# Kernel optimization log

Hardware: AMD Instinct MI355X
Metric: run time of the kernel (lower is better)

The kernel has to match this reference:

```python
import jax, jax.numpy as jnp
import numpy as np

EMBED_DIM = 1024
NUM_HEADS = 16
HEAD_DIM = EMBED_DIM // NUM_HEADS
B, S = 4, 2048


def setup_inputs() -> dict:
    key = jax.random.key(0)
    ks = jax.random.split(key, 12)
    s = 1.0 / np.sqrt(EMBED_DIM)
    inp = {
        'q': jax.random.normal(ks[0], (B, S, EMBED_DIM), jnp.float32),
        'k': jax.random.normal(ks[1], (B, S, EMBED_DIM), jnp.float32),
        'v': jax.random.normal(ks[2], (B, S, EMBED_DIM), jnp.float32),
        'mask': jnp.tril(jnp.ones((S, S), jnp.int32))[None, None],  # [1,1,S,S] causal
        'Wq': jax.random.normal(ks[3], (EMBED_DIM, EMBED_DIM), jnp.float32) * s,
        'bq': jax.random.normal(ks[4], (EMBED_DIM,), jnp.float32) * s,
        'Wk': jax.random.normal(ks[5], (EMBED_DIM, EMBED_DIM), jnp.float32) * s,
        'bk': jax.random.normal(ks[6], (EMBED_DIM,), jnp.float32) * s,
        'Wv': jax.random.normal(ks[7], (EMBED_DIM, EMBED_DIM), jnp.float32) * s,
        'bv': jax.random.normal(ks[8], (EMBED_DIM,), jnp.float32) * s,
        'Wo': jax.random.normal(ks[9], (EMBED_DIM, EMBED_DIM), jnp.float32) * s,
        'bo': jax.random.normal(ks[10], (EMBED_DIM,), jnp.float32) * s,
    }
    return inp


def _split(x):
    b, s, _ = x.shape
    return x.reshape(b, s, NUM_HEADS, HEAD_DIM).transpose(0, 2, 1, 3)  # [b,h,s,d]


def reference(q, k, v, mask, Wq, bq, Wk, bk, Wv, bv, Wo, bo):
    # torch Linear: x @ W.T + b
    Q = _split(q @ Wq.T + bq)
    K = _split(k @ Wk.T + bk)
    V = _split(v @ Wv.T + bv)
    scores = jnp.einsum('bhqd,bhkd->bhqk', Q, K) / np.sqrt(HEAD_DIM).astype(np.float32)
    scores = jnp.where(mask == 0, jnp.float32(-1e9), scores)
    attn = jax.nn.softmax(scores, axis=-1)  # dropout p=0.0 -> identity
    out = jnp.einsum('bhqk,bhkd->bhqd', attn, V)
    out = out.transpose(0, 2, 1, 3).reshape(q.shape[0], q.shape[1], EMBED_DIM)
    return out @ Wo.T + bo
```

## Files before the change

### kernel.cpp

```cpp
#include <hip/hip_runtime.h>

#define SEQ   2048
#define EMB   1024
#define NH    16
#define HD    64
#define BATCH 4

typedef __attribute__((ext_vector_type(8))) short short8;
typedef __attribute__((ext_vector_type(4))) float floatx4;
typedef __attribute__((ext_vector_type(4))) uint uintx4;

static __device__ __forceinline__ ushort f2bf_rne(float x) {
  unsigned u = __float_as_uint(x);
  unsigned r = u + 0x7FFFu + ((u >> 16) & 1u);
  return (ushort)(r >> 16);
}
static __device__ __forceinline__ float bf2f(ushort h) {
  return __uint_as_float(((unsigned)h) << 16);
}

static __device__ __forceinline__ uint pk_bf16(float a, float b) {
  uint r;
  asm("v_cvt_pk_bf16_f32 %0, %1, %2" : "=v"(r) : "v"(a), "v"(b));
  return r;
}
static __device__ __forceinline__ void split_pair(float a, float b, uint& h,
                                                  uint& l) {
  h = pk_bf16(a, b);
  const float ha = __uint_as_float(h << 16);
  const float hb = __uint_as_float(h & 0xFFFF0000u);
  l = pk_bf16(a - ha, b - hb);
}

static __device__ __forceinline__ void load16(const void* g, void* l) {
  __builtin_amdgcn_global_load_lds(
      (const __attribute__((address_space(1))) unsigned int*)g,
      (__attribute__((address_space(3))) unsigned int*)l, 16, 0, 0);
}

static __device__ __forceinline__ int swz_off(int row, int kg) {
  return (row >> 1) * 128 + (((row & 1) << 2) + (kg ^ ((row >> 1) & 3))) * 16;
}

static __device__ __forceinline__ void stage_tile(const ushort* __restrict__ g,
                                                  int row0, int k0,
                                                  ushort* lds, int t) {
#pragma unroll
  for (int i = 0; i < 2; ++i) {
    const int slot = t + i * 256;
    const int line = slot >> 3, s = slot & 7;
    const int row = line * 2 + (s >> 2);
    const int c = (s & 3) ^ (line & 3);
    load16(g + (size_t)(row0 + row) * EMB + k0 + c * 8, lds + slot * 8);
  }
}

static __device__ __forceinline__ void wconv_body(const float* W, ushort* Yh,
                                                  ushort* Yl, int bid, int t) {
  const int i = (bid * 256 + t) * 8;
  const float4 a = *(const float4*)(W + i);
  const float4 b = *(const float4*)(W + i + 4);
  const float xv[8] = {a.x, a.y, a.z, a.w, b.x, b.y, b.z, b.w};
  uintx4 H, L;
#pragma unroll
  for (int j = 0; j < 4; ++j) {
    uint h, l;
    split_pair(xv[2 * j], xv[2 * j + 1], h, l);
    H[j] = h;
    L[j] = l;
  }
  *(uintx4*)&Yh[i] = H;
  *(uintx4*)&Yl[i] = L;
}

__global__ __launch_bounds__(256) void wconv4_kernel(
    const float* __restrict__ Wq, const float* __restrict__ Wk,
    const float* __restrict__ Wv, const float* __restrict__ Wo,
    ushort* __restrict__ Yqh, ushort* __restrict__ Yql,
    ushort* __restrict__ Ykh, ushort* __restrict__ Ykl,
    ushort* __restrict__ Yvh, ushort* __restrict__ Yvl,
    ushort* __restrict__ Yoh, ushort* __restrict__ Yol) {
  const int which = blockIdx.x >> 9;
  const int bid = blockIdx.x & 511;
  const float* W = which == 0 ? Wq : which == 1 ? Wk : which == 2 ? Wv : Wo;
  ushort* Yh = which == 0 ? Yqh : which == 1 ? Ykh : which == 2 ? Yvh : Yoh;
  ushort* Yl = which == 0 ? Yql : which == 1 ? Ykl : which == 2 ? Yvl : Yol;
  wconv_body(W, Yh, Yl, bid, threadIdx.x);
}

__global__ __launch_bounds__(256) void wconv3_kernel(
    const float* __restrict__ Wq, const float* __restrict__ Wk,
    const float* __restrict__ Wv, ushort* __restrict__ Yqh,
    ushort* __restrict__ Yql, ushort* __restrict__ Ykh,
    ushort* __restrict__ Ykl, ushort* __restrict__ Yvh,
    ushort* __restrict__ Yvl) {
  const int which = blockIdx.x >> 9;
  const int bid = blockIdx.x & 511;
  const float* W = which == 0 ? Wq : which == 1 ? Wk : Wv;
  ushort* Yh = which == 0 ? Yqh : which == 1 ? Ykh : Yvh;
  ushort* Yl = which == 0 ? Yql : which == 1 ? Ykl : Yvl;
  wconv_body(W, Yh, Yl, bid, threadIdx.x);
}

__global__ __launch_bounds__(256) void wconv_kernel(const float* __restrict__ W,
                                                    ushort* __restrict__ Yh,
                                                    ushort* __restrict__ Yl) {
  wconv_body(W, Yh, Yl, blockIdx.x, threadIdx.x);
}

__global__ __launch_bounds__(256) void qkv_proj_kernel(
    const float* __restrict__ Xq, const float* __restrict__ Xk,
    const float* __restrict__ Xv, const ushort* __restrict__ Wqh,
    const ushort* __restrict__ Wql, const ushort* __restrict__ Wkh,
    const ushort* __restrict__ Wkl, const ushort* __restrict__ Wvh,
    const ushort* __restrict__ Wvl, const float* __restrict__ bq,
    const float* __restrict__ bk, const float* __restrict__ bv,
    ushort* __restrict__ Qh, ushort* __restrict__ Ql, ushort* __restrict__ Kh,
    ushort* __restrict__ Kl, ushort* __restrict__ Vth,
    ushort* __restrict__ Vtl) {
  __shared__ ushort Ahi[2][128 * 40], Alo[2][128 * 40];
  __shared__ ushort Bhi[2][128 * 32], Blo[2][128 * 32];

  const int mode = blockIdx.z;
  const float* X = mode == 0 ? Xq : mode == 1 ? Xk : Xv;
  const ushort* Wh = mode == 0 ? Wqh : mode == 1 ? Wkh : Wvh;
  const ushort* Wl = mode == 0 ? Wql : mode == 1 ? Wkl : Wvl;
  const float* bias = mode == 0 ? bq : mode == 1 ? bk : bv;
  ushort* Yh = mode == 0 ? Qh : mode == 1 ? Kh : Vth;
  ushort* Yl = mode == 0 ? Ql : mode == 1 ? Kl : Vtl;

  const int t = threadIdx.x;
  const int lane = t & 63, wave = t >> 6;
  const int m0 = blockIdx.y * 128, n0 = blockIdx.x * 128;
  const int wm = (wave >> 1) * 64, wn = (wave & 1) * 64;
  const int fr = lane & 15, kg = lane >> 4;

  floatx4 acc[4][4];
#pragma unroll
  for (int i = 0; i < 4; ++i)
#pragma unroll
    for (int j = 0; j < 4; ++j)
#pragma unroll
      for (int r = 0; r < 4; ++r) acc[i][j][r] = 0.f;

  auto stageB = [&](int k0, int b) {
    stage_tile(Wh, n0, k0, Bhi[b], t);
    stage_tile(Wl, n0, k0, Blo[b], t);
  };
  auto stageA = [&](int k0, int b) {
#pragma unroll
    for (int i = 0; i < 4; ++i) {
      const int f = t + 256 * i;
      const int row = f >> 3, kq = f & 7;
      const float4 v =
          *(const float4*)(X + (size_t)(m0 + row) * EMB + k0 + kq * 4);
      uint h0, l0, h1, l1;
      split_pair(v.x, v.y, h0, l0);
      split_pair(v.z, v.w, h1, l1);
      uint2 hp, lp;
      hp.x = h0; hp.y = h1;
      lp.x = l0; lp.y = l1;
      *(uint2*)&Ahi[b][row * 40 + kq * 4] = hp;
      *(uint2*)&Alo[b][row * 40 + kq * 4] = lp;
    }
  };
  auto computeStep = [&](int cur) {
    short8 bhv[4], blv[4];
#pragma unroll
    for (int nf = 0; nf < 4; ++nf) {
      const int row = wn + nf * 16 + fr;
      const int off = swz_off(row, kg);
      bhv[nf] = *(const short8*)((const char*)Bhi[cur] + off);
      blv[nf] = *(const short8*)((const char*)Blo[cur] + off);
    }
#pragma unroll
    for (int mf = 0; mf < 4; ++mf) {
      const int arow = wm + mf * 16 + fr;
      const short8 ah = *(const short8*)&Ahi[cur][arow * 40 + kg * 8];
      const short8 al = *(const short8*)&Alo[cur][arow * 40 + kg * 8];
#pragma unroll
      for (int nf = 0; nf < 4; ++nf) {
        acc[mf][nf] = __builtin_amdgcn_mfma_f32_16x16x32_bf16(ah, bhv[nf],
                                                              acc[mf][nf], 0, 0, 0);
        acc[mf][nf] = __builtin_amdgcn_mfma_f32_16x16x32_bf16(ah, blv[nf],
                                                              acc[mf][nf], 0, 0, 0);
        acc[mf][nf] = __builtin_amdgcn_mfma_f32_16x16x32_bf16(al, bhv[nf],
                                                              acc[mf][nf], 0, 0, 0);
      }
    }
  };

  stageB(0, 0);
  stageA(0, 0);
  asm volatile("s_waitcnt vmcnt(0)");
  __syncthreads();
#pragma unroll 1
  for (int k0 = 0; k0 < EMB; k0 += 32) {
    const int cur = (k0 >> 5) & 1;
    if (k0 + 32 < EMB) {
      stageB(k0 + 32, cur ^ 1);
      stageA(k0 + 32, cur ^ 1);
    }
    computeStep(cur);
    asm volatile("s_waitcnt vmcnt(0)");
    __syncthreads();
  }

  const int rg = lane >> 4;
#pragma unroll
  for (int nf = 0; nf < 4; ++nf) {
    const int n = n0 + wn + nf * 16 + fr;
    const float bb = bias[n];
    if (mode == 2) {
      const int hh = n >> 6, d = n & 63;
#pragma unroll
      for (int mf = 0; mf < 4; ++mf) {
        const int mb = m0 + wm + mf * 16 + rg * 4;
        const int b = mb >> 11, s = mb & (SEQ - 1);
        uint h0, l0, h1, l1;
        split_pair(acc[mf][nf][0] + bb, acc[mf][nf][1] + bb, h0, l0);
        split_pair(acc[mf][nf][2] + bb, acc[mf][nf][3] + bb, h1, l1);
        uint2 hp, lp;
        hp.x = h0; hp.y = h1;
        lp.x = l0; lp.y = l1;
        const int idx = (b * NH + hh) * (HD * SEQ) + d * SEQ + s;
        *(uint2*)&Yh[idx] = hp;
        *(uint2*)&Yl[idx] = lp;
      }
    } else {
      const float scaleq = (mode == 0) ? 0.125f : 1.0f;
#pragma unroll
      for (int mf = 0; mf < 4; ++mf) {
#pragma unroll
        for (int r = 0; r < 4; ++r) {
          const int m = m0 + wm + mf * 16 + rg * 4 + r;
          const float val = (acc[mf][nf][r] + bb) * scaleq;
          const int hh = n >> 6, d = n & 63;
          const int b = m >> 11, s = m & (SEQ - 1);
          const int idx = ((b * NH + hh) * SEQ + s) * HD + d;
          const ushort h = f2bf_rne(val);
          Yh[idx] = h;
          Yl[idx] = f2bf_rne(val - bf2f(h));
        }
      }
    }
  }
}

template <int MODE, bool PREA, bool PREB>
__global__ __launch_bounds__(256) void proj_mfma_kernel(
    const float* __restrict__ X, const ushort* __restrict__ Xh,
    const ushort* __restrict__ Xl, const float* __restrict__ W,
    const ushort* __restrict__ Wh, const ushort* __restrict__ Wl,
    const float* __restrict__ bias, float* __restrict__ Yf,
    ushort* __restrict__ Yh, ushort* __restrict__ Yl) {
  constexpr bool DBUF = (PREA || PREB);
  constexpr int NB = DBUF ? 2 : 1;
  constexpr int ASZ = PREA ? 128 * 32 : 128 * 40;
  constexpr int BSZ = PREB ? 128 * 32 : 128 * 40;
  __shared__ ushort Ahi[NB][ASZ], Alo[NB][ASZ];
  __shared__ ushort Bhi[NB][BSZ], Blo[NB][BSZ];

  const int t = threadIdx.x;
  const int lane = t & 63, wave = t >> 6;
  const int m0 = blockIdx.y * 128, n0 = blockIdx.x * 128;
  const int wm = (wave >> 1) * 64, wn = (wave & 1) * 64;
  const int fr = lane & 15, kg = lane >> 4;

  floatx4 acc[4][4];
#pragma unroll
  for (int i = 0; i < 4; ++i)
#pragma unroll
    for (int j = 0; j < 4; ++j)
#pragma unroll
      for (int r = 0; r < 4; ++r) acc[i][j][r] = 0.f;

  auto stageB = [&](int k0, int b) {
    if constexpr (PREB) {
      stage_tile(Wh, n0, k0, Bhi[b], t);
      stage_tile(Wl, n0, k0, Blo[b], t);
    } else {
#pragma unroll
      for (int i = 0; i < 4; ++i) {
        const int f = t + 256 * i;
        const int row = f >> 3, kq = f & 7;
        const float4 v =
            *(const float4*)(W + (size_t)(n0 + row) * EMB + k0 + kq * 4);
        uint h0, l0, h1, l1;
        split_pair(v.x, v.y, h0, l0);
        split_pair(v.z, v.w, h1, l1);
        uint2 hp, lp;
        hp.x = h0; hp.y = h1;
        lp.x = l0; lp.y = l1;
        *(uint2*)&Bhi[b][row * 40 + kq * 4] = hp;
        *(uint2*)&Blo[b][row * 40 + kq * 4] = lp;
      }
    }
  };
  auto stageA = [&](int k0, int b) {
    if constexpr (PREA) {
      stage_tile(Xh, m0, k0, Ahi[b], t);
      stage_tile(Xl, m0, k0, Alo[b], t);
    } else {
#pragma unroll
      for (int i = 0; i < 4; ++i) {
        const int f = t + 256 * i;
        const int row = f >> 3, kq = f & 7;
        const float4 v =
            *(const float4*)(X + (size_t)(m0 + row) * EMB + k0 + kq * 4);
        uint h0, l0, h1, l1;
        split_pair(v.x, v.y, h0, l0);
        split_pair(v.z, v.w, h1, l1);
        uint2 hp, lp;
        hp.x = h0; hp.y = h1;
        lp.x = l0; lp.y = l1;
        *(uint2*)&Ahi[b][row * 40 + kq * 4] = hp;
        *(uint2*)&Alo[b][row * 40 + kq * 4] = lp;
      }
    }
  };
  auto computeStep = [&](int cur) {
    short8 bhv[4], blv[4];
#pragma unroll
    for (int nf = 0; nf < 4; ++nf) {
      const int row = wn + nf * 16 + fr;
      if constexpr (PREB) {
        const int off = swz_off(row, kg);
        bhv[nf] = *(const short8*)((const char*)Bhi[cur] + off);
        blv[nf] = *(const short8*)((const char*)Blo[cur] + off);
      } else {
        bhv[nf] = *(const short8*)&Bhi[cur][row * 40 + kg * 8];
        blv[nf] = *(const short8*)&Blo[cur][row * 40 + kg * 8];
      }
    }
#pragma unroll
    for (int mf = 0; mf < 4; ++mf) {
      const int arow = wm + mf * 16 + fr;
      short8 ah, al;
      if constexpr (PREA) {
        const int off = swz_off(arow, kg);
        ah = *(const short8*)((const char*)Ahi[cur] + off);
        al = *(const short8*)((const char*)Alo[cur] + off);
      } else {
        ah = *(const short8*)&Ahi[cur][arow * 40 + kg * 8];
        al = *(const short8*)&Alo[cur][arow * 40 + kg * 8];
      }
#pragma unroll
      for (int nf = 0; nf < 4; ++nf) {
        acc[mf][nf] = __builtin_amdgcn_mfma_f32_16x16x32_bf16(ah, bhv[nf],
                                                              acc[mf][nf], 0, 0, 0);
        acc[mf][nf] = __builtin_amdgcn_mfma_f32_16x16x32_bf16(ah, blv[nf],
                                                              acc[mf][nf], 0, 0, 0);
        acc[mf][nf] = __builtin_amdgcn_mfma_f32_16x16x32_bf16(al, bhv[nf],
                                                              acc[mf][nf], 0, 0, 0);
      }
    }
  };

  if constexpr (DBUF) {
    stageB(0, 0);
    stageA(0, 0);
    asm volatile("s_waitcnt vmcnt(0)");
    __syncthreads();
#pragma unroll 1
    for (int k0 = 0; k0 < EMB; k0 += 32) {
      const int cur = (k0 >> 5) & 1;
      if (k0 + 32 < EMB) {
        stageB(k0 + 32, cur ^ 1);
        stageA(k0 + 32, cur ^ 1);
      }
      computeStep(cur);
      asm volatile("s_waitcnt vmcnt(0)");
      __syncthreads();
    }
  } else {
#pragma unroll 1
    for (int k0 = 0; k0 < EMB; k0 += 32) {
      __syncthreads();
      stageB(k0, 0);
      stageA(k0, 0);
      __syncthreads();
      computeStep(0);
    }
  }

  const int rg = lane >> 4;
#pragma unroll
  for (int nf = 0; nf < 4; ++nf) {
    const int n = n0 + wn + nf * 16 + fr;
    const float bb = bias[n];
    if (MODE == 2) {
      const int hh = n >> 6, d = n & 63;
#pragma unroll
      for (int mf = 0; mf < 4; ++mf) {
        const int mb = m0 + wm + mf * 16 + rg * 4;
        const int b = mb >> 11, s = mb & (SEQ - 1);
        uint h0, l0, h1, l1;
        split_pair(acc[mf][nf][0] + bb, acc[mf][nf][1] + bb, h0, l0);
        split_pair(acc[mf][nf][2] + bb, acc[mf][nf][3] + bb, h1, l1);
        uint2 hp, lp;
        hp.x = h0; hp.y = h1;
        lp.x = l0; lp.y = l1;
        const int idx = (b * NH + hh) * (HD * SEQ) + d * SEQ + s;
        *(uint2*)&Yh[idx] = hp;
        *(uint2*)&Yl[idx] = lp;
      }
    } else {
#pragma unroll
      for (int mf = 0; mf < 4; ++mf) {
#pragma unroll
        for (int r = 0; r < 4; ++r) {
          const int m = m0 + wm + mf * 16 + rg * 4 + r;
          float val = acc[mf][nf][r] + bb;
          if (MODE == 3) {
            Yf[(size_t)m * EMB + n] = val;
          } else {
            if (MODE == 0) val *= 0.125f;
            const int hh = n >> 6, d = n & 63;
            const int b = m >> 11, s = m & (SEQ - 1);
            const int idx = ((b * NH + hh) * SEQ + s) * HD + d;
            const ushort h = f2bf_rne(val);
            Yh[idx] = h;
            Yl[idx] = f2bf_rne(val - bf2f(h));
          }
        }
      }
    }
  }
}

template <bool SPLITOUT>
__global__ __launch_bounds__(256, 2) void attn_mfma_kernel(
    const ushort* __restrict__ Qh, const ushort* __restrict__ Ql,
    const ushort* __restrict__ Kh, const ushort* __restrict__ Kl,
    const ushort* __restrict__ Vth, const ushort* __restrict__ Vtl,
    float* __restrict__ O, ushort* __restrict__ Oh, ushort* __restrict__ Ol) {
  __shared__ __align__(16) ushort KHs[2][64 * 64], KLs[2][64 * 64];
  __shared__ __align__(16) ushort VHs[2][64 * 64], VLs[2][64 * 64];

  const int bh = blockIdx.x;
  const int qtA = blockIdx.y;
  const int qtB = 15 - qtA;
  const int t = threadIdx.x;
  const int lane = t & 63, wave = t >> 6;
  const int fr = lane & 15, kg = lane >> 4;
  const int base = bh * (SEQ * HD);
  const int r8 = lane >> 3, c8 = lane & 7;

  const int q00[2] = {qtA * 128 + wave * 32, qtB * 128 + wave * 32};
  const int ext[2] = {(q00[0] + 95) >> 6, (q00[1] + 95) >> 6};
  const int nkt = 2 * qtB + 2;

  short8 qfh[2][2][2], qfl[2][2][2];
#pragma unroll
  for (int g = 0; g < 2; ++g)
#pragma unroll
    for (int mf = 0; mf < 2; ++mf)
#pragma unroll
      for (int ks = 0; ks < 2; ++ks) {
        const int idx = base + (q00[g] + mf * 16 + fr) * HD + ks * 32 + kg * 8;
        qfh[g][mf][ks] = *(const short8*)&Qh[idx];
        qfl[g][mf][ks] = *(const short8*)&Ql[idx];
      }

  floatx4 oacc[2][2][4];
  float m_run[2][2], l_run[2][2];
#pragma unroll
  for (int g = 0; g < 2; ++g)
#pragma unroll
    for (int mf = 0; mf < 2; ++mf) {
#pragma unroll
      for (int nf = 0; nf < 4; ++nf)
#pragma unroll
        for (int r = 0; r < 4; ++r) oacc[g][mf][nf][r] = 0.f;
      m_run[g][mf] = -INFINITY;
      l_run[g][mf] = 0.f;
    }

  auto stage = [&](int kt, int b) {
#pragma unroll
    for (int i = 0; i < 2; ++i) {
      const int lrow = wave * 16 + i * 8;
      const int row = lrow + r8;
      const int sw = (c8 ^ (row & 7)) << 3;
      const int gk = base + (kt * 64 + row) * HD + sw;
      const int gv = base + row * SEQ + kt * 64 + sw;
      load16(Kh + gk, (char*)KHs + b * 8192 + lrow * 128);
      load16(Kl + gk, (char*)KLs + b * 8192 + lrow * 128);
      load16(Vth + gv, (char*)VHs + b * 8192 + lrow * 128);
      load16(Vtl + gv, (char*)VLs + b * 8192 + lrow * 128);
    }
  };

  stage(0, 0);
  asm volatile("s_waitcnt vmcnt(0)");
  __syncthreads();

#pragma unroll 1
  for (int kt = 0; kt < nkt; ++kt) {
    const int cur = kt & 1;
    if (kt + 1 < nkt) stage(kt + 1, cur ^ 1);
    const int c0 = kt * 64;
    const int kb = cur * 8192;

#pragma unroll
    for (int g = 0; g < 2; ++g) {
      if (kt < ext[g]) {
        const int q0 = q00[g];

        floatx4 s2[2][4];
#pragma unroll
        for (int mf = 0; mf < 2; ++mf)
#pragma unroll
          for (int nf = 0; nf < 4; ++nf)
#pragma unroll
            for (int r = 0; r < 4; ++r) s2[mf][nf][r] = 0.f;

#pragma unroll
        for (int ksd = 0; ksd < 2; ++ksd)
#pragma unroll
          for (int nf = 0; nf < 4; ++nf) {
            const int kr =
                32 * (nf >> 1) + 8 * (fr >> 2) + 4 * (nf & 1) + (fr & 3);
            const int byo = kb + kr * 128 + (((ksd * 4 + kg) ^ (kr & 7)) << 4);
            const short8 kh = *(const short8*)((const char*)KHs + byo);
            const short8 kl = *(const short8*)((const char*)KLs + byo);
#pragma unroll
            for (int mf = 0; mf < 2; ++mf) {
              s2[mf][nf] = __builtin_amdgcn_mfma_f32_16x16x32_bf16(
                  kh, qfh[g][mf][ksd], s2[mf][nf], 0, 0, 0);
              s2[mf][nf] = __builtin_amdgcn_mfma_f32_16x16x32_bf16(
                  kh, qfl[g][mf][ksd], s2[mf][nf], 0, 0, 0);
              s2[mf][nf] = __builtin_amdgcn_mfma_f32_16x16x32_bf16(
                  kl, qfh[g][mf][ksd], s2[mf][nf], 0, 0, 0);
            }
          }

        if (c0 + 63 > q0) {
#pragma unroll
          for (int mf = 0; mf < 2; ++mf)
#pragma unroll
            for (int nf = 0; nf < 4; ++nf)
#pragma unroll
              for (int r = 0; r < 4; ++r) {
                const int col =
                    c0 + 32 * (nf >> 1) + 8 * kg + 4 * (nf & 1) + r;
                const int row = q0 + mf * 16 + fr;
                if (col > row) s2[mf][nf][r] = -1e9f;
              }
        }

        float pmv[2];
#pragma unroll
        for (int mf = 0; mf < 2; ++mf) {
          float pm = s2[mf][0][0];
#pragma unroll
          for (int nf = 0; nf < 4; ++nf)
#pragma unroll
            for (int r = 0; r < 4; ++r) pm = fmaxf(pm, s2[mf][nf][r]);
          pm = fmaxf(pm, __shfl_xor(pm, 16));
          pm = fmaxf(pm, __shfl_xor(pm, 32));
          pmv[mf] = pm;
        }
        float alpha2[2] = {1.f, 1.f};
        const bool grow = !__all((pmv[0] <= m_run[g][0] + 8.f) &&
                                 (pmv[1] <= m_run[g][1] + 8.f));
        if (grow) {
#pragma unroll
          for (int mf = 0; mf < 2; ++mf) {
            const float mnew = fmaxf(m_run[g][mf], pmv[mf]);
            alpha2[mf] = __expf(m_run[g][mf] - mnew);
            m_run[g][mf] = mnew;
          }
#pragma unroll
          for (int mf = 0; mf < 2; ++mf)
#pragma unroll
            for (int r = 0; r < 4; ++r) {
              const float a = __shfl(alpha2[mf], (kg * 4 + r) | (lane & 48));
#pragma unroll
              for (int nf = 0; nf < 4; ++nf) oacc[g][mf][nf][r] *= a;
            }
        }
#pragma unroll
        for (int mf = 0; mf < 2; ++mf) {
          const float mm = m_run[g][mf];
          float sum = 0.f;
#pragma unroll
          for (int nf = 0; nf < 4; ++nf)
#pragma unroll
            for (int r = 0; r < 4; ++r) {
              const float p = __expf(s2[mf][nf][r] - mm);
              s2[mf][nf][r] = p;
              sum += p;
            }
          sum += __shfl_xor(sum, 16);
          sum += __shfl_xor(sum, 32);
          l_run[g][mf] = l_run[g][mf] * alpha2[mf] + sum;
        }

        short8 pah[2][2], pal[2][2];
#pragma unroll
        for (int mf = 0; mf < 2; ++mf)
#pragma unroll
          for (int ks = 0; ks < 2; ++ks) {
            uintx4 H, L;
#pragma unroll
            for (int jj = 0; jj < 4; ++jj) {
              const int nfi = 2 * ks + (jj >> 1);
              uint h, l;
              split_pair(s2[mf][nfi][(2 * jj) & 3], s2[mf][nfi][(2 * jj + 1) & 3],
                         h, l);
              H[jj] = h;
              L[jj] = l;
            }
            pah[mf][ks] = *(short8*)&H;
            pal[mf][ks] = *(short8*)&L;
          }

#pragma unroll
        for (int ks = 0; ks < 2; ++ks)
#pragma unroll
          for (int nf = 0; nf < 4; ++nf) {
            const int d = nf * 16 + fr;
            const int byo = kb + d * 128 + (((ks * 4 + kg) ^ (d & 7)) << 4);
            const short8 vh = *(const short8*)((const char*)VHs + byo);
            const short8 vl = *(const short8*)((const char*)VLs + byo);
#pragma unroll
            for (int mf = 0; mf < 2; ++mf) {
              oacc[g][mf][nf] = __builtin_amdgcn_mfma_f32_16x16x32_bf16(
                  pah[mf][ks], vh, oacc[g][mf][nf], 0, 0, 0);
              oacc[g][mf][nf] = __builtin_amdgcn_mfma_f32_16x16x32_bf16(
                  pah[mf][ks], vl, oacc[g][mf][nf], 0, 0, 0);
              oacc[g][mf][nf] = __builtin_amdgcn_mfma_f32_16x16x32_bf16(
                  pal[mf][ks], vh, oacc[g][mf][nf], 0, 0, 0);
            }
          }
      }
    }

    asm volatile("s_waitcnt vmcnt(0)");
    __syncthreads();
  }

  const int b = bh >> 4, hsel = bh & 15;
#pragma unroll
  for (int g = 0; g < 2; ++g)
#pragma unroll
    for (int mf = 0; mf < 2; ++mf)
#pragma unroll
      for (int r = 0; r < 4; ++r) {
        const float lv = __shfl(l_run[g][mf], (kg * 4 + r) | (lane & 48));
        const float inv = 1.f / lv;
        const int grow2 = q00[g] + mf * 16 + kg * 4 + r;
        const int rowbase = (b * SEQ + grow2) * EMB + hsel * HD;
#pragma unroll
        for (int nf = 0; nf < 4; ++nf) {
          const float val = oacc[g][mf][nf][r] * inv;
          const int idx = rowbase + nf * 16 + fr;
          if constexpr (SPLITOUT) {
            const ushort hh = f2bf_rne(val);
            Oh[idx] = hh;
            Ol[idx] = f2bf_rne(val - bf2f(hh));
          } else {
            O[idx] = val;
          }
        }
      }
}

extern "C" void kernel_launch(void* const* d_in, const int* in_sizes, int n_in,
                              void* d_out, int out_size, void* d_ws,
                              size_t ws_size, hipStream_t stream) {
  const float* q = (const float*)d_in[0];
  const float* k = (const float*)d_in[1];
  const float* v = (const float*)d_in[2];
  const float* Wq = (const float*)d_in[4];
  const float* bq = (const float*)d_in[5];
  const float* Wk = (const float*)d_in[6];
  const float* bk = (const float*)d_in[7];
  const float* Wv = (const float*)d_in[8];
  const float* bv = (const float*)d_in[9];
  const float* Wo = (const float*)d_in[10];
  const float* bo = (const float*)d_in[11];
  float* out = (float*)d_out;

  const size_t E = (size_t)BATCH * SEQ * EMB;
  const size_t WE = (size_t)EMB * EMB;
  ushort* us = (ushort*)d_ws;
  ushort* Qh = us;
  ushort* Ql = us + E;
  ushort* Kh = us + 2 * E;
  ushort* Kl = us + 3 * E;
  ushort* Vth = us + 4 * E;
  ushort* Vtl = us + 5 * E;

  const dim3 pgrid(EMB / 128, (BATCH * SEQ) / 128);
  const dim3 qgrid(EMB / 128, (BATCH * SEQ) / 128, 3);
  const dim3 agrid(BATCH * NH, 8);
  const dim3 blk(256);
  const int wgrid = (int)(WE / 8 / 256);

  if (ws_size >= (8 * E + 2 * WE) * sizeof(ushort)) {
    ushort* W3 = us + 6 * E;
    ushort* Wqh = W3, *Wql = W3 + WE;
    ushort* Wkh = W3 + 2 * WE, *Wkl = W3 + 3 * WE;
    ushort* Wvh = W3 + 4 * WE, *Wvl = W3 + 5 * WE;
    ushort* Woh = us + 8 * E, *Wol = us + 8 * E + WE;
    ushort* AOh = us + 6 * E, *AOl = us + 7 * E;

    wconv4_kernel<<<4 * wgrid, blk, 0, stream>>>(Wq, Wk, Wv, Wo, Wqh, Wql, Wkh,
                                                 Wkl, Wvh, Wvl, Woh, Wol);
    qkv_proj_kernel<<<qgrid, blk, 0, stream>>>(q, k, v, Wqh, Wql, Wkh, Wkl,
                                               Wvh, Wvl, bq, bk, bv, Qh, Ql,
                                               Kh, Kl, Vth, Vtl);
    attn_mfma_kernel<true><<<agrid, blk, 0, stream>>>(Qh, Ql, Kh, Kl, Vth, Vtl,
                                                      nullptr, AOh, AOl);
    proj_mfma_kernel<3, true, true><<<pgrid, blk, 0, stream>>>(
        nullptr, AOh, AOl, nullptr, Woh, Wol, bo, out, nullptr, nullptr);
  } else if (ws_size >= 8 * E * sizeof(ushort)) {
    ushort* W3 = us + 6 * E;
    ushort* Wqh = W3, *Wql = W3 + WE;
    ushort* Wkh = W3 + 2 * WE, *Wkl = W3 + 3 * WE;
    ushort* Wvh = W3 + 4 * WE, *Wvl = W3 + 5 * WE;
    ushort* AOh = us + 6 * E, *AOl = us + 7 * E;
    ushort* Woh = us, *Wol = us + WE;

    wconv3_kernel<<<3 * wgrid, blk, 0, stream>>>(Wq, Wk, Wv, Wqh, Wql, Wkh,
                                                 Wkl, Wvh, Wvl);
    qkv_proj_kernel<<<qgrid, blk, 0, stream>>>(q, k, v, Wqh, Wql, Wkh, Wkl,
                                               Wvh, Wvl, bq, bk, bv, Qh, Ql,
                                               Kh, Kl, Vth, Vtl);
    attn_mfma_kernel<true><<<agrid, blk, 0, stream>>>(Qh, Ql, Kh, Kl, Vth, Vtl,
                                                      nullptr, AOh, AOl);
    wconv_kernel<<<wgrid, blk, 0, stream>>>(Wo, Woh, Wol);
    proj_mfma_kernel<3, true, true><<<pgrid, blk, 0, stream>>>(
        nullptr, AOh, AOl, nullptr, Woh, Wol, bo, out, nullptr, nullptr);
  } else if (ws_size >= (6 * E + 6 * WE) * sizeof(ushort)) {
    ushort* W3 = us + 6 * E;
    ushort* Wqh = W3, *Wql = W3 + WE;
    ushort* Wkh = W3 + 2 * WE, *Wkl = W3 + 3 * WE;
    ushort* Wvh = W3 + 4 * WE, *Wvl = W3 + 5 * WE;
    ushort* AOh = (ushort*)d_out, *AOl = AOh + E;
    ushort* Woh = us, *Wol = us + WE;
    float* PO = (float*)(us + 2 * E);

    wconv3_kernel<<<3 * wgrid, blk, 0, stream>>>(Wq, Wk, Wv, Wqh, Wql, Wkh,
                                                 Wkl, Wvh, Wvl);
    qkv_proj_kernel<<<qgrid, blk, 0, stream>>>(q, k, v, Wqh, Wql, Wkh, Wkl,
                                               Wvh, Wvl, bq, bk, bv, Qh, Ql,
                                               Kh, Kl, Vth, Vtl);
    attn_mfma_kernel<true><<<agrid, blk, 0, stream>>>(Qh, Ql, Kh, Kl, Vth, Vtl,
                                                      nullptr, AOh, AOl);
    wconv_kernel<<<wgrid, blk, 0, stream>>>(Wo, Woh, Wol);
    proj_mfma_kernel<3, true, true><<<pgrid, blk, 0, stream>>>(
        nullptr, AOh, AOl, nullptr, Woh, Wol, bo, PO, nullptr, nullptr);
    hipError_t e1 = hipMemcpyAsync(out, PO, E * sizeof(float),
                                   hipMemcpyDeviceToDevice, stream);
    (void)e1;
  } else {
    float* AO = out;
    float* PO = (float*)d_ws;
    proj_mfma_kernel<0, false, false><<<pgrid, blk, 0, stream>>>(
        q, nullptr, nullptr, Wq, nullptr, nullptr, bq, nullptr, Qh, Ql);
    proj_mfma_kernel<1, false, false><<<pgrid, blk, 0, stream>>>(
        k, nullptr, nullptr, Wk, nullptr, nullptr, bk, nullptr, Kh, Kl);
    proj_mfma_kernel<2, false, false><<<pgrid, blk, 0, stream>>>(
        v, nullptr, nullptr, Wv, nullptr, nullptr, bv, nullptr, Vth, Vtl);
    attn_mfma_kernel<false><<<agrid, blk, 0, stream>>>(
        Qh, Ql, Kh, Kl, Vth, Vtl, AO, nullptr, nullptr);
    proj_mfma_kernel<3, false, false><<<pgrid, blk, 0, stream>>>(
        AO, nullptr, nullptr, Wo, nullptr, nullptr, bo, PO, nullptr, nullptr);
    hipError_t e2 = hipMemcpyAsync(out, PO, E * sizeof(float),
                                   hipMemcpyDeviceToDevice, stream);
    (void)e2;
  }
}
```

Baseline: 365.1 us.

## Triple-buffer weight tiles and split A global loads from LDS writes in projections

The QKV and output projection GEMMs now keep three LDS buffers for the pre-split weight tiles, prefetching two K-steps ahead with a partial vmcnt wait instead of draining all loads each step. In the QKV kernel the fp32 activation loads go into registers before the B prefetch is issued and are converted and written to LDS afterwards, and the A tile uses an XOR swizzle in place of row padding. The output projection becomes a dedicated kernel with the same deeper pipeline, and the fallback paths move to a separate legacy kernel. This costs more LDS per block, which may lower occupancy, and the partial vmcnt counts depend on exactly how many loads stage_tile issues.

After: 370.6 us. No clear change (+1.5%).

```diff
diff --git a/kernel.cpp b/kernel.cpp
--- a/kernel.cpp
+++ b/kernel.cpp
@@ -118,8 +118,8 @@
     ushort* __restrict__ Qh, ushort* __restrict__ Ql, ushort* __restrict__ Kh,
     ushort* __restrict__ Kl, ushort* __restrict__ Vth,
     ushort* __restrict__ Vtl) {
-  __shared__ ushort Ahi[2][128 * 40], Alo[2][128 * 40];
-  __shared__ ushort Bhi[2][128 * 32], Blo[2][128 * 32];
+  __shared__ ushort Ahi[2][128 * 32], Alo[2][128 * 32];
+  __shared__ ushort Bhi[3][128 * 32], Blo[3][128 * 32];
 
   const int mode = blockIdx.z;
   const float* X = mode == 0 ? Xq : mode == 1 ? Xk : Xv;
@@ -147,37 +147,45 @@
     stage_tile(Wh, n0, k0, Bhi[b], t);
     stage_tile(Wl, n0, k0, Blo[b], t);
   };
-  auto stageA = [&](int k0, int b) {
+  auto loadA_regs = [&](int k0, float4* xr) {
 #pragma unroll
     for (int i = 0; i < 4; ++i) {
       const int f = t + 256 * i;
       const int row = f >> 3, kq = f & 7;
-      const float4 v =
-          *(const float4*)(X + (size_t)(m0 + row) * EMB + k0 + kq * 4);
+      xr[i] = *(const float4*)(X + (size_t)(m0 + row) * EMB + k0 + kq * 4);
+    }
+  };
+  auto writeA_regs = [&](const float4* xr, int b) {
+#pragma unroll
+    for (int i = 0; i < 4; ++i) {
+      const int f = t + 256 * i;
+      const int row = f >> 3, kq = f & 7;
+      const int kqp = (((kq >> 1) ^ ((row >> 1) & 3)) << 1) + (kq & 1);
       uint h0, l0, h1, l1;
-      split_pair(v.x, v.y, h0, l0);
-      split_pair(v.z, v.w, h1, l1);
+      split_pair(xr[i].x, xr[i].y, h0, l0);
+      split_pair(xr[i].z, xr[i].w, h1, l1);
       uint2 hp, lp;
       hp.x = h0; hp.y = h1;
       lp.x = l0; lp.y = l1;
-      *(uint2*)&Ahi[b][row * 40 + kq * 4] = hp;
-      *(uint2*)&Alo[b][row * 40 + kq * 4] = lp;
+      *(uint2*)&Ahi[b][row * 32 + kqp * 4] = hp;
+      *(uint2*)&Alo[b][row * 32 + kqp * 4] = lp;
     }
   };
-  auto computeStep = [&](int cur) {
+  auto computeStep = [&](int cb, int ca) {
     short8 bhv[4], blv[4];
 #pragma unroll
     for (int nf = 0; nf < 4; ++nf) {
       const int row = wn + nf * 16 + fr;
-      const int off = swz_off(row, kg);
-      bhv[nf] = *(const short8*)((const char*)Bhi[cur] + off);
-      blv[nf] = *(const short8*)((const char*)Blo[cur] + off);
+      const int off = cb * 8192 + swz_off(row, kg);
+      bhv[nf] = *(const short8*)((const char*)Bhi + off);
+      blv[nf] = *(const short8*)((const char*)Blo + off);
     }
 #pragma unroll
     for (int mf = 0; mf < 4; ++mf) {
       const int arow = wm + mf * 16 + fr;
-      const short8 ah = *(const short8*)&Ahi[cur][arow * 40 + kg * 8];
-      const short8 al = *(const short8*)&Alo[cur][arow * 40 + kg * 8];
+      const int pch = kg ^ ((arow >> 1) & 3);
+      const short8 ah = *(const short8*)&Ahi[ca][arow * 32 + pch * 8];
+      const short8 al = *(const short8*)&Alo[ca][arow * 32 + pch * 8];
 #pragma unroll
       for (int nf = 0; nf < 4; ++nf) {
         acc[mf][nf] = __builtin_amdgcn_mfma_f32_16x16x32_bf16(ah, bhv[nf],
@@ -190,19 +198,30 @@
     }
   };
 
-  stageB(0, 0);
-  stageA(0, 0);
-  asm volatile("s_waitcnt vmcnt(0)");
+  {
+    float4 xr0[4];
+    loadA_regs(0, xr0);
+    stageB(0, 0);
+    stageB(32, 1);
+    writeA_regs(xr0, 0);
+  }
+  asm volatile("s_waitcnt vmcnt(4)");
   __syncthreads();
+
 #pragma unroll 1
   for (int k0 = 0; k0 < EMB; k0 += 32) {
-    const int cur = (k0 >> 5) & 1;
-    if (k0 + 32 < EMB) {
-      stageB(k0 + 32, cur ^ 1);
-      stageA(k0 + 32, cur ^ 1);
-    }
-    computeStep(cur);
-    asm volatile("s_waitcnt vmcnt(0)");
+    const int step = k0 >> 5;
+    const int cb = step % 3, ca = step & 1;
+    const bool mA = (k0 + 32 < EMB), mB = (k0 + 64 < EMB);
+    float4 xr[4];
+    if (mA) loadA_regs(k0 + 32, xr);
+    if (mB) stageB(k0 + 64, (step + 2) % 3);
+    if (mA) writeA_regs(xr, ca ^ 1);
+    computeStep(cb, ca);
+    if (mB)
+      asm volatile("s_waitcnt vmcnt(4)");
+    else
+      asm volatile("s_waitcnt vmcnt(0)");
     __syncthreads();
   }
 
@@ -247,19 +266,12 @@
   }
 }
 
-template <int MODE, bool PREA, bool PREB>
-__global__ __launch_bounds__(256) void proj_mfma_kernel(
-    const float* __restrict__ X, const ushort* __restrict__ Xh,
-    const ushort* __restrict__ Xl, const float* __restrict__ W,
+__global__ __launch_bounds__(256) void oproj_mfma_kernel(
+    const ushort* __restrict__ Xh, const ushort* __restrict__ Xl,
     const ushort* __restrict__ Wh, const ushort* __restrict__ Wl,
-    const float* __restrict__ bias, float* __restrict__ Yf,
-    ushort* __restrict__ Yh, ushort* __restrict__ Yl) {
-  constexpr bool DBUF = (PREA || PREB);
-  constexpr int NB = DBUF ? 2 : 1;
-  constexpr int ASZ = PREA ? 128 * 32 : 128 * 40;
-  constexpr int BSZ = PREB ? 128 * 32 : 128 * 40;
-  __shared__ ushort Ahi[NB][ASZ], Alo[NB][ASZ];
-  __shared__ ushort Bhi[NB][BSZ], Blo[NB][BSZ];
+    const float* __restrict__ bias, float* __restrict__ Yf) {
+  __shared__ ushort Ahi[2][128 * 32], Alo[2][128 * 32];
+  __shared__ ushort Bhi[3][128 * 32], Blo[3][128 * 32];
 
   const int t = threadIdx.x;
   const int lane = t & 63, wave = t >> 6;
@@ -275,15 +287,120 @@
 #pragma unroll
       for (int r = 0; r < 4; ++r) acc[i][j][r] = 0.f;
 
+  auto stageA = [&](int k0, int b) {
+    stage_tile(Xh, m0, k0, Ahi[b], t);
+    stage_tile(Xl, m0, k0, Alo[b], t);
+  };
   auto stageB = [&](int k0, int b) {
-    if constexpr (PREB) {
-      stage_tile(Wh, n0, k0, Bhi[b], t);
-      stage_tile(Wl, n0, k0, Blo[b], t);
-    } else {
-#pragma unroll
-      for (int i = 0; i < 4; ++i) {
-        const int f = t + 256 * i;
-        const int row = f >> 3, kq = f & 7;
+    stage_tile(Wh, n0, k0, Bhi[b], t);
+    stage_tile(Wl, n0, k0, Blo[b], t);
+  };
+  auto computeStep = [&](int cb, int ca) {
+    short8 bhv[4], blv[4];
+#pragma unroll
+    for (int nf = 0; nf < 4; ++nf) {
+      const int row = wn + nf * 16 + fr;
+      const int off = cb * 8192 + swz_off(row, kg);
+      bhv[nf] = *(const short8*)((const char*)Bhi + off);
+      blv[nf] = *(const short8*)((const char*)Blo + off);
+    }
+#pragma unroll
+    for (int mf = 0; mf < 4; ++mf) {
+      const int arow = wm + mf * 16 + fr;
+      const int offa = ca * 8192 + swz_off(arow, kg);
+      const short8 ah = *(const short8*)((const char*)Ahi + offa);
+      const short8 al = *(const short8*)((const char*)Alo + offa);
+#pragma unroll
+      for (int nf = 0; nf < 4; ++nf) {
+        acc[mf][nf] = __builtin_amdgcn_mfma_f32_16x16x32_bf16(ah, bhv[nf],
+                                                              acc[mf][nf], 0, 0, 0);
+        acc[mf][nf] = __builtin_amdgcn_mfma_f32_16x16x32_bf16(ah, blv[nf],
+                                                              acc[mf][nf], 0, 0, 0);
+        acc[mf][nf] = __builtin_amdgcn_mfma_f32_16x16x32_bf16(al, bhv[nf],
+                                                              acc[mf][nf], 0, 0, 0);
+      }
+    }
+  };
+
+  stageA(0, 0);
+  stageB(0, 0);
+  stageB(32, 1);
+  asm volatile("s_waitcnt vmcnt(4)");
+  __syncthreads();
+
+#pragma unroll 1
+  for (int k0 = 0; k0 < EMB; k0 += 32) {
+    const int step = k0 >> 5;
+    const int cb = step % 3, ca = step & 1;
+    const bool mA = (k0 + 32 < EMB), mB = (k0 + 64 < EMB);
+    if (mA) stageA(k0 + 32, ca ^ 1);
+    if (mB) stageB(k0 + 64, (step + 2) % 3);
+    computeStep(cb, ca);
+    if (mB)
+      asm volatile("s_waitcnt vmcnt(4)");
+    else
+      asm volatile("s_waitcnt vmcnt(0)");
+    __syncthreads();
+  }
+
+  const int rg = lane >> 4;
+#pragma unroll
+  for (int nf = 0; nf < 4; ++nf) {
+    const int n = n0 + wn + nf * 16 + fr;
+    const float bb = bias[n];
+#pragma unroll
+    for (int mf = 0; mf < 4; ++mf) {
+#pragma unroll
+      for (int r = 0; r < 4; ++r) {
+        const int m = m0 + wm + mf * 16 + rg * 4 + r;
+        Yf[(size_t)m * EMB + n] = acc[mf][nf][r] + bb;
+      }
+    }
+  }
+}
+
+template <int MODE>
+__global__ __launch_bounds__(256) void legacy_proj_kernel(
+    const float* __restrict__ X, const float* __restrict__ W,
+    const float* __restrict__ bias, float* __restrict__ Yf,
+    ushort* __restrict__ Yh, ushort* __restrict__ Yl) {
+  __shared__ ushort Ahi[128 * 40], Alo[128 * 40];
+  __shared__ ushort Bhi[128 * 40], Blo[128 * 40];
+
+  const int t = threadIdx.x;
+  const int lane = t & 63, wave = t >> 6;
+  const int m0 = blockIdx.y * 128, n0 = blockIdx.x * 128;
+  const int wm = (wave >> 1) * 64, wn = (wave & 1) * 64;
+  const int fr = lane & 15, kg = lane >> 4;
+
+  floatx4 acc[4][4];
+#pragma unroll
+  for (int i = 0; i < 4; ++i)
+#pragma unroll
+    for (int j = 0; j < 4; ++j)
+#pragma unroll
+      for (int r = 0; r < 4; ++r) acc[i][j][r] = 0.f;
+
+#pragma unroll 1
+  for (int k0 = 0; k0 < EMB; k0 += 32) {
+    __syncthreads();
+#pragma unroll
+    for (int i = 0; i < 4; ++i) {
+      const int f = t + 256 * i;
+      const int row = f >> 3, kq = f & 7;
+      {
+        const float4 v =
+            *(const float4*)(X + (size_t)(m0 + row) * EMB + k0 + kq * 4);
+        uint h0, l0, h1, l1;
+        split_pair(v.x, v.y, h0, l0);
+        split_pair(v.z, v.w, h1, l1);
+        uint2 hp, lp;
+        hp.x = h0; hp.y = h1;
+        lp.x = l0; lp.y = l1;
+        *(uint2*)&Ahi[row * 40 + kq * 4] = hp;
+        *(uint2*)&Alo[row * 40 + kq * 4] = lp;
+      }
+      {
         const float4 v =
             *(const float4*)(W + (size_t)(n0 + row) * EMB + k0 + kq * 4);
         uint h0, l0, h1, l1;
@@ -292,59 +409,24 @@
         uint2 hp, lp;
         hp.x = h0; hp.y = h1;
         lp.x = l0; lp.y = l1;
-        *(uint2*)&Bhi[b][row * 40 + kq * 4] = hp;
-        *(uint2*)&Blo[b][row * 40 + kq * 4] = lp;
-      }
-    }
-  };
-  auto stageA = [&](int k0, int b) {
-    if constexpr (PREA) {
-      stage_tile(Xh, m0, k0, Ahi[b], t);
-      stage_tile(Xl, m0, k0, Alo[b], t);
-    } else {
-#pragma unroll
-      for (int i = 0; i < 4; ++i) {
-        const int f = t + 256 * i;
-        const int row = f >> 3, kq = f & 7;
-        const float4 v =
-            *(const float4*)(X + (size_t)(m0 + row) * EMB + k0 + kq * 4);
-        uint h0, l0, h1, l1;
-        split_pair(v.x, v.y, h0, l0);
-        split_pair(v.z, v.w, h1, l1);
-        uint2 hp, lp;
-        hp.x = h0; hp.y = h1;
-        lp.x = l0; lp.y = l1;
-        *(uint2*)&Ahi[b][row * 40 + kq * 4] = hp;
-        *(uint2*)&Alo[b][row * 40 + kq * 4] = lp;
-      }
-    }
-  };
-  auto computeStep = [&](int cur) {
+        *(uint2*)&Bhi[row * 40 + kq * 4] = hp;
+        *(uint2*)&Blo[row * 40 + kq * 4] = lp;
+      }
+    }
+    __syncthreads();
+
     short8 bhv[4], blv[4];
 #pragma unroll
     for (int nf = 0; nf < 4; ++nf) {
       const int row = wn + nf * 16 + fr;
-      if constexpr (PREB) {
-        const int off = swz_off(row, kg);
-        bhv[nf] = *(const short8*)((const char*)Bhi[cur] + off);
-        blv[nf] = *(const short8*)((const char*)Blo[cur] + off);
-      } else {
-        bhv[nf] = *(const short8*)&Bhi[cur][row * 40 + kg * 8];
-        blv[nf] = *(const short8*)&Blo[cur][row * 40 + kg * 8];
-      }
+      bhv[nf] = *(const short8*)&Bhi[row * 40 + kg * 8];
+      blv[nf] = *(const short8*)&Blo[row * 40 + kg * 8];
     }
 #pragma unroll
     for (int mf = 0; mf < 4; ++mf) {
       const int arow = wm + mf * 16 + fr;
-      short8 ah, al;
-      if constexpr (PREA) {
-        const int off = swz_off(arow, kg);
-        ah = *(const short8*)((const char*)Ahi[cur] + off);
-        al = *(const short8*)((const char*)Alo[cur] + off);
-      } else {
-        ah = *(const short8*)&Ahi[cur][arow * 40 + kg * 8];
-        al = *(const short8*)&Alo[cur][arow * 40 + kg * 8];
-      }
+      const short8 ah = *(const short8*)&Ahi[arow * 40 + kg * 8];
+      const short8 al = *(const short8*)&Alo[arow * 40 + kg * 8];
 #pragma unroll
       for (int nf = 0; nf < 4; ++nf) {
         acc[mf][nf] = __builtin_amdgcn_mfma_f32_16x16x32_bf16(ah, bhv[nf],
@@ -354,33 +436,6 @@
         acc[mf][nf] = __builtin_amdgcn_mfma_f32_16x16x32_bf16(al, bhv[nf],
                                                               acc[mf][nf], 0, 0, 0);
       }
-    }
-  };
-
-  if constexpr (DBUF) {
-    stageB(0, 0);
-    stageA(0, 0);
-    asm volatile("s_waitcnt vmcnt(0)");
-    __syncthreads();
-#pragma unroll 1
-    for (int k0 = 0; k0 < EMB; k0 += 32) {
-      const int cur = (k0 >> 5) & 1;
-      if (k0 + 32 < EMB) {
-        stageB(k0 + 32, cur ^ 1);
-        stageA(k0 + 32, cur ^ 1);
-      }
-      computeStep(cur);
-      asm volatile("s_waitcnt vmcnt(0)");
-      __syncthreads();
-    }
-  } else {
-#pragma unroll 1
-    for (int k0 = 0; k0 < EMB; k0 += 32) {
-      __syncthreads();
-      stageB(k0, 0);
-      stageA(k0, 0);
-      __syncthreads();
-      computeStep(0);
     }
   }
 
@@ -715,8 +770,7 @@
                                                Kh, Kl, Vth, Vtl);
     attn_mfma_kernel<true><<<agrid, blk, 0, stream>>>(Qh, Ql, Kh, Kl, Vth, Vtl,
                                                       nullptr, AOh, AOl);
-    proj_mfma_kernel<3, true, true><<<pgrid, blk, 0, stream>>>(
-        nullptr, AOh, AOl, nullptr, Woh, Wol, bo, out, nullptr, nullptr);
+    oproj_mfma_kernel<<<pgrid, blk, 0, stream>>>(AOh, AOl, Woh, Wol, bo, out);
   } else if (ws_size >= 8 * E * sizeof(ushort)) {
     ushort* W3 = us + 6 * E;
     ushort* Wqh = W3, *Wql = W3 + WE;
@@ -733,8 +787,7 @@
     attn_mfma_kernel<true><<<agrid, blk, 0, stream>>>(Qh, Ql, Kh, Kl, Vth, Vtl,
                                                       nullptr, AOh, AOl);
     wconv_kernel<<<wgrid, blk, 0, stream>>>(Wo, Woh, Wol);
-    proj_mfma_kernel<3, true, true><<<pgrid, blk, 0, stream>>>(
-        nullptr, AOh, AOl, nullptr, Woh, Wol, bo, out, nullptr, nullptr);
+    oproj_mfma_kernel<<<pgrid, blk, 0, stream>>>(AOh, AOl, Woh, Wol, bo, out);
   } else if (ws_size >= (6 * E + 6 * WE) * sizeof(ushort)) {
     ushort* W3 = us + 6 * E;
     ushort* Wqh = W3, *Wql = W3 + WE;
@@ -752,24 +805,23 @@
     attn_mfma_kernel<true><<<agrid, blk, 0, stream>>>(Qh, Ql, Kh, Kl, Vth, Vtl,
                                                       nullptr, AOh, AOl);
     wconv_kernel<<<wgrid, blk, 0, stream>>>(Wo, Woh, Wol);
-    proj_mfma_kernel<3, true, true><<<pgrid, blk, 0, stream>>>(
-        nullptr, AOh, AOl, nullptr, Woh, Wol, bo, PO, nullptr, nullptr);
+    oproj_mfma_kernel<<<pgrid, blk, 0, stream>>>(AOh, AOl, Woh, Wol, bo, PO);
     hipError_t e1 = hipMemcpyAsync(out, PO, E * sizeof(float),
                                    hipMemcpyDeviceToDevice, stream);
     (void)e1;
   } else {
     float* AO = out;
     float* PO = (float*)d_ws;
-    proj_mfma_kernel<0, false, false><<<pgrid, blk, 0, stream>>>(
-        q, nullptr, nullptr, Wq, nullptr, nullptr, bq, nullptr, Qh, Ql);
-    proj_mfma_kernel<1, false, false><<<pgrid, blk, 0, stream>>>(
-        k, nullptr, nullptr, Wk, nullptr, nullptr, bk, nullptr, Kh, Kl);
-    proj_mfma_kernel<2, false, false><<<pgrid, blk, 0, stream>>>(
-        v, nullptr, nullptr, Wv, nullptr, nullptr, bv, nullptr, Vth, Vtl);
+    legacy_proj_kernel<0><<<pgrid, blk, 0, stream>>>(q, Wq, bq, nullptr, Qh,
+                                                     Ql);
+    legacy_proj_kernel<1><<<pgrid, blk, 0, stream>>>(k, Wk, bk, nullptr, Kh,
+                                                     Kl);
+    legacy_proj_kernel<2><<<pgrid, blk, 0, stream>>>(v, Wv, bv, nullptr, Vth,
+                                                     Vtl);
     attn_mfma_kernel<false><<<agrid, blk, 0, stream>>>(
         Qh, Ql, Kh, Kl, Vth, Vtl, AO, nullptr, nullptr);
-    proj_mfma_kernel<3, false, false><<<pgrid, blk, 0, stream>>>(
-        AO, nullptr, nullptr, Wo, nullptr, nullptr, bo, PO, nullptr, nullptr);
+    legacy_proj_kernel<3><<<pgrid, blk, 0, stream>>>(AO, Wo, bo, PO, nullptr,
+                                                     nullptr);
     hipError_t e2 = hipMemcpyAsync(out, PO, E * sizeof(float),
                                    hipMemcpyDeviceToDevice, stream);
     (void)e2;
```
